# Kernel optimization log

Hardware: AMD Instinct MI355X
Metric: run time of the kernel (lower is better)

Reference implementation:

```python
import jax, jax.numpy as jnp
import numpy as np
import math

CHANNELS = 128
NUM_NODES = 170
LENGTH = 12
BATCH = 128


def setup_inputs() -> dict:
    key = jax.random.key(0)
    k_x, k_es = jax.random.split(key)
    x = jax.random.normal(k_x, (BATCH, CHANNELS, NUM_NODES, LENGTH), dtype=jnp.float32)
    # xavier_uniform for E_s [channels, num_nodes]
    bound = math.sqrt(6.0 / (CHANNELS + NUM_NODES))
    E_s = jax.random.uniform(k_es, (CHANNELS, NUM_NODES), dtype=jnp.float32,
                             minval=-bound, maxval=bound)
    return {"x": x, "E_s": E_s}


def reference(x, E_s):
    # x: [B, C, N, T], E_s: [C, M] with M == N (num_nodes)
    # Note: the original also computes E_t = x * E_tod**2, which is dead code
    # (never used in the returned value), so it is omitted here.
    C = x.shape[1]
    # node embeddings: sum over channel and time -> [B, N, M]
    E_d = jnp.tanh(jnp.einsum('bcnt,cm->bnm', x, E_s))
    # node-node similarity: contract over the M (embedding) axis -> [B, N, N]
    scores = jax.nn.relu(jnp.einsum('bnm,bkm->bnk', E_d, E_d) / jnp.sqrt(jnp.float32(C)))
    A_adp = jax.nn.softmax(scores, axis=-1)  # [B, N, N]
    A_mean = A_adp.mean(axis=0)              # [N, N]
    return (A_mean > 0.5).astype(jnp.float32)
```

## Files before the change

kernel.cpp:

```cpp
#include <hip/hip_runtime.h>
#include <math.h>

#define NB 128
#define NC 128
#define NN 170
#define NT 12
#define MP 176
#define BSROW 196

#define ED_SZ ((size_t)NB * NN * MP)
#define P_SZ  ((size_t)NB * NN * MP)

typedef _Float16 h8 __attribute__((ext_vector_type(8)));
typedef _Float16 h4 __attribute__((ext_vector_type(4)));
typedef __fp16   g2 __attribute__((ext_vector_type(2)));
typedef float    f4 __attribute__((ext_vector_type(4)));

__device__ __forceinline__ float fast_tanh(float x) {
    float cx = fminf(fmaxf(x, -15.f), 15.f);
    float e  = __expf(2.f * cx);
    return (e - 1.f) * __builtin_amdgcn_rcpf(e + 1.f);
}

__global__ __launch_bounds__(256) void k2_fused(const float* __restrict__ x,
                                                const float* __restrict__ Es,
                                                _Float16* __restrict__ Ed) {
    const int b = blockIdx.y, n0 = blockIdx.x * 32;
    const int t = threadIdx.x, tx = t & 15, ty = t >> 4;
    __shared__ __align__(16) float As[16][36];
    __shared__ __align__(16) float Bs[16][BSROW];

    float acc[2][12] = {};
    for (int c0 = 0; c0 < NC; c0 += 16) {
        __syncthreads();
        {
            int c  = t >> 4;
            int nn = (t & 15) * 2;
            #pragma unroll
            for (int u = 0; u < 2; ++u) {
                int n = n0 + nn + u;
                float s = 0.f;
                if (n < NN) {
                    const float4* p = reinterpret_cast<const float4*>(
                        x + ((size_t)((b * NC + c0 + c) * NN) + n) * NT);
                    float4 f0 = p[0], f1 = p[1], f2 = p[2];
                    s = ((f0.x + f0.y) + (f0.z + f0.w))
                      + ((f1.x + f1.y) + (f1.z + f1.w))
                      + ((f2.x + f2.y) + (f2.z + f2.w));
                }
                As[c][nn + u] = s;
            }
        }
        #pragma unroll
        for (int it = 0; it < 11; ++it) {
            int idx = t + it * 256;
            int c = idx / 176, m = idx - c * 176;
            Bs[c][m] = (m < NN) ? Es[(c0 + c) * NN + m] : 0.f;
        }
        __syncthreads();
        #pragma unroll
        for (int cc = 0; cc < 16; ++cc) {
            float2 av = *reinterpret_cast<const float2*>(&As[cc][ty * 2]);
            float a[2] = {av.x, av.y};
            float bb[12];
            #pragma unroll
            for (int off = 0; off < 3; ++off) {
                float4 bv = *reinterpret_cast<const float4*>(&Bs[cc][tx * 4 + off * 64]);
                bb[off * 4 + 0] = bv.x; bb[off * 4 + 1] = bv.y;
                bb[off * 4 + 2] = bv.z; bb[off * 4 + 3] = bv.w;
            }
            #pragma unroll
            for (int ii = 0; ii < 2; ++ii)
                #pragma unroll
                for (int jj = 0; jj < 12; ++jj)
                    acc[ii][jj] = fmaf(a[ii], bb[jj], acc[ii][jj]);
        }
    }
    #pragma unroll
    for (int ii = 0; ii < 2; ++ii) {
        int n = n0 + ty * 2 + ii;
        if (n >= NN) continue;
        _Float16* Erow = Ed + ((size_t)(b * NN + n)) * MP;
        #pragma unroll
        for (int off = 0; off < 3; ++off) {
            int m = tx * 4 + off * 64;
            if (m >= MP) continue;
            g2 lo = __builtin_amdgcn_cvt_pkrtz(fast_tanh(acc[ii][off * 4 + 0]),
                                               fast_tanh(acc[ii][off * 4 + 1]));
            g2 hi = __builtin_amdgcn_cvt_pkrtz(fast_tanh(acc[ii][off * 4 + 2]),
                                               fast_tanh(acc[ii][off * 4 + 3]));
            h4 hv;
            hv[0] = (_Float16)lo[0]; hv[1] = (_Float16)lo[1];
            hv[2] = (_Float16)hi[0]; hv[3] = (_Float16)hi[1];
            *reinterpret_cast<h4*>(Erow + m) = hv;
        }
    }
}

__global__ __launch_bounds__(256) void k3_scores_mfma(const _Float16* __restrict__ Ed,
                                                      _Float16* __restrict__ P) {
    const int b = blockIdx.y, r0 = blockIdx.x * 32;
    const int t = threadIdx.x;
    const int lane = t & 63, wave = t >> 6;
    const int l15 = lane & 15, quad = lane >> 4;

    __shared__ __align__(16) _Float16 Eh[192 * 40];
    __shared__ __align__(16) float    Sc[32 * 204];

    const _Float16* __restrict__ Edb = Ed + (size_t)b * NN * MP;

    f4 acc[2][3] = {};
    for (int mc = 0; mc < 192; mc += 32) {
        __syncthreads();
        #pragma unroll
        for (int it = 0; it < 3; ++it) {
            int idx = t + it * 256;
            int row = idx >> 2, q = idx & 3;
            int col = mc + q * 8;
            h8 v = {};
            if (row < NN && col < MP)
                v = *reinterpret_cast<const h8*>(Edb + (size_t)row * MP + col);
            *reinterpret_cast<h8*>(&Eh[row * 40 + q * 8]) = v;
        }
        __syncthreads();
        const int ko = quad * 8;
        h8 a0 = *reinterpret_cast<const h8*>(&Eh[(r0 + l15) * 40 + ko]);
        h8 a1 = *reinterpret_cast<const h8*>(&Eh[(r0 + 16 + l15) * 40 + ko]);
        #pragma unroll
        for (int ci = 0; ci < 3; ++ci) {
            int kc = (wave * 3 + ci) * 16 + l15;
            h8 bf = *reinterpret_cast<const h8*>(&Eh[kc * 40 + ko]);
            acc[0][ci] = __builtin_amdgcn_mfma_f32_16x16x32_f16(a0, bf, acc[0][ci], 0, 0, 0);
            acc[1][ci] = __builtin_amdgcn_mfma_f32_16x16x32_f16(a1, bf, acc[1][ci], 0, 0, 0);
        }
    }

    const float scale = 0.08838834764831845f;
    #pragma unroll
    for (int rt = 0; rt < 2; ++rt)
        #pragma unroll
        for (int ci = 0; ci < 3; ++ci) {
            int col = (wave * 3 + ci) * 16 + l15;
            #pragma unroll
            for (int reg = 0; reg < 4; ++reg) {
                int rloc = rt * 16 + quad * 4 + reg;
                Sc[rloc * 204 + col] = fmaxf(acc[rt][ci][reg] * scale, 0.f);
            }
        }
    __syncthreads();

    for (int rr = 0; rr < 8; ++rr) {
        int r = wave * 8 + rr;
        int n = r0 + r;
        if (n >= NN) continue;
        float v0 = Sc[r * 204 + lane];
        float v1 = Sc[r * 204 + lane + 64];
        int  k2i = lane + 128;
        bool has2 = (k2i < NN);
        float v2 = has2 ? Sc[r * 204 + k2i] : -1.f;
        float m = fmaxf(fmaxf(v0, v1), v2);
        #pragma unroll
        for (int off = 32; off; off >>= 1) m = fmaxf(m, __shfl_xor(m, off, 64));
        float e0 = __expf(v0 - m);
        float e1 = __expf(v1 - m);
        float e2 = has2 ? __expf(v2 - m) : 0.f;
        float s = e0 + e1 + e2;
        #pragma unroll
        for (int off = 32; off; off >>= 1) s += __shfl_xor(s, off, 64);
        float inv = 1.f / s;
        _Float16* Pr = P + ((size_t)(b * NN + n)) * MP;
        Pr[lane]      = (_Float16)(e0 * inv);
        Pr[lane + 64] = (_Float16)(e1 * inv);
        if (has2) Pr[k2i] = (_Float16)(e2 * inv);
    }
}

__global__ __launch_bounds__(256) void k4_mean_thresh(const _Float16* __restrict__ P,
                                                      float* __restrict__ out) {
    int p = blockIdx.x * 256 + threadIdx.x;
    if (p >= NN * NN) return;
    int n = p / NN, k = p - n * NN;
    const _Float16* base = P + (size_t)n * MP + k;
    float s0 = 0.f, s1 = 0.f, s2 = 0.f, s3 = 0.f;
    #pragma unroll
    for (int b = 0; b < NB; b += 4) {
        s0 += (float)base[(size_t)(b + 0) * NN * MP];
        s1 += (float)base[(size_t)(b + 1) * NN * MP];
        s2 += (float)base[(size_t)(b + 2) * NN * MP];
        s3 += (float)base[(size_t)(b + 3) * NN * MP];
    }
    float s = (s0 + s1) + (s2 + s3);
    out[p] = (s * (1.f / 128.f) > 0.5f) ? 1.f : 0.f;
}

extern "C" void kernel_launch(void* const* d_in, const int* in_sizes, int n_in,
                              void* d_out, int out_size, void* d_ws, size_t ws_size,
                              hipStream_t stream) {
    const float* x  = (const float*)d_in[0];
    const float* Es = (const float*)d_in[1];
    float* out = (float*)d_out;

    _Float16* Ed = (_Float16*)d_ws;
    _Float16* P  = Ed + ED_SZ;

    k2_fused<<<dim3(6, 128), 256, 0, stream>>>(x, Es, Ed);
    k3_scores_mfma<<<dim3(6, 128), 256, 0, stream>>>(Ed, P);
    k4_mean_thresh<<<113, 256, 0, stream>>>(P, out);
}
```

Before: 253.9 us.

## Split time-sum into separate kernel and compute E_d with fp16 MFMA

The fused fp32 FMA kernel for E_d is replaced by three kernels: a transpose and fp16 conversion of E_s, a coalesced kernel that sums x over time into an fp16 buffer, and an MFMA 16x16x32 kernel that computes the channel contraction and applies tanh. The aim is to read x with fully coalesced, simple loads and move the matmul onto matrix cores instead of scalar FMAs. The cost is two extra launches, an extra global round trip for the time-summed x, fp16 rounding of the sums and of E_s, and scalar fp16 stores for E_d.

```diff
diff --git a/kernel.cpp b/kernel.cpp
--- a/kernel.cpp
+++ b/kernel.cpp
@@ -6,10 +6,12 @@
 #define NN 170
 #define NT 12
 #define MP 176
-#define BSROW 196
-
-#define ED_SZ ((size_t)NB * NN * MP)
-#define P_SZ  ((size_t)NB * NN * MP)
+#define MEST 192
+
+#define EST_SZ ((size_t)MEST * NC)
+#define XS_SZ  ((size_t)NB * NC * NN)
+#define ED_SZ  ((size_t)NB * NN * MP)
+#define P_SZ   ((size_t)NB * NN * MP)
 
 typedef _Float16 h8 __attribute__((ext_vector_type(8)));
 typedef _Float16 h4 __attribute__((ext_vector_type(4)));
@@ -22,79 +24,83 @@
     return (e - 1.f) * __builtin_amdgcn_rcpf(e + 1.f);
 }
 
-__global__ __launch_bounds__(256) void k2_fused(const float* __restrict__ x,
-                                                const float* __restrict__ Es,
-                                                _Float16* __restrict__ Ed) {
+__global__ __launch_bounds__(256) void k0t_transpose_es(const float* __restrict__ Es,
+                                                        _Float16* __restrict__ Est) {
+    int idx = blockIdx.x * 256 + threadIdx.x;
+    if (idx >= MEST * NC) return;
+    int m = idx >> 7, c = idx & 127;
+    Est[idx] = (m < NN) ? (_Float16)Es[c * NN + m] : (_Float16)0.f;
+}
+
+__global__ __launch_bounds__(256) void k1_tsum(const float* __restrict__ x,
+                                               _Float16* __restrict__ xs) {
+    unsigned tid = blockIdx.x * 256 + threadIdx.x;
+    unsigned bc = tid / 85u;
+    unsigned p  = tid - bc * 85u;
+    const float4* q = reinterpret_cast<const float4*>(
+        x + (size_t)bc * (NN * NT) + (size_t)p * (2 * NT));
+    float4 f0 = q[0], f1 = q[1], f2 = q[2];
+    float4 f3 = q[3], f4v = q[4], f5 = q[5];
+    float s0 = ((f0.x + f0.y) + (f0.z + f0.w))
+             + ((f1.x + f1.y) + (f1.z + f1.w))
+             + ((f2.x + f2.y) + (f2.z + f2.w));
+    float s1 = ((f3.x + f3.y) + (f3.z + f3.w))
+             + ((f4v.x + f4v.y) + (f4v.z + f4v.w))
+             + ((f5.x + f5.y) + (f5.z + f5.w));
+    g2 pk = __builtin_amdgcn_cvt_pkrtz(s0, s1);
+    *reinterpret_cast<g2*>(xs + (size_t)bc * NN + 2 * p) = pk;
+}
+
+__global__ __launch_bounds__(256) void k2_ed_mfma(const _Float16* __restrict__ xs,
+                                                  const _Float16* __restrict__ Est,
+                                                  _Float16* __restrict__ Ed) {
     const int b = blockIdx.y, n0 = blockIdx.x * 32;
-    const int t = threadIdx.x, tx = t & 15, ty = t >> 4;
-    __shared__ __align__(16) float As[16][36];
-    __shared__ __align__(16) float Bs[16][BSROW];
-
-    float acc[2][12] = {};
-    for (int c0 = 0; c0 < NC; c0 += 16) {
-        __syncthreads();
-        {
-            int c  = t >> 4;
-            int nn = (t & 15) * 2;
+    const int t = threadIdx.x;
+    const int lane = t & 63, wave = t >> 6;
+    const int l15 = lane & 15, quad = lane >> 4;
+
+    __shared__ __align__(16) _Float16 At[32 * 40];
+
+    const _Float16* __restrict__ xsb = xs + (size_t)b * NC * NN;
+
+    f4 acc[2][3] = {};
+    for (int c0 = 0; c0 < NC; c0 += 32) {
+        __syncthreads();
+        #pragma unroll
+        for (int it = 0; it < 4; ++it) {
+            int slot = t + it * 256;
+            int c = slot >> 5, n = slot & 31;
+            _Float16 v = (_Float16)0.f;
+            if (n0 + n < NN)
+                v = xsb[(size_t)(c0 + c) * NN + n0 + n];
+            At[n * 40 + c] = v;
+        }
+        __syncthreads();
+        const int ko = quad * 8;
+        h8 a0 = *reinterpret_cast<const h8*>(&At[l15 * 40 + ko]);
+        h8 a1 = *reinterpret_cast<const h8*>(&At[(16 + l15) * 40 + ko]);
+        #pragma unroll
+        for (int ci = 0; ci < 3; ++ci) {
+            int kc = (wave * 3 + ci) * 16 + l15;
+            h8 bf = *reinterpret_cast<const h8*>(Est + (size_t)kc * NC + c0 + ko);
+            acc[0][ci] = __builtin_amdgcn_mfma_f32_16x16x32_f16(a0, bf, acc[0][ci], 0, 0, 0);
+            acc[1][ci] = __builtin_amdgcn_mfma_f32_16x16x32_f16(a1, bf, acc[1][ci], 0, 0, 0);
+        }
+    }
+
+    #pragma unroll
+    for (int rt = 0; rt < 2; ++rt)
+        #pragma unroll
+        for (int ci = 0; ci < 3; ++ci) {
+            int m = (wave * 3 + ci) * 16 + l15;
+            if (m >= MP) continue;
             #pragma unroll
-            for (int u = 0; u < 2; ++u) {
-                int n = n0 + nn + u;
-                float s = 0.f;
-                if (n < NN) {
-                    const float4* p = reinterpret_cast<const float4*>(
-                        x + ((size_t)((b * NC + c0 + c) * NN) + n) * NT);
-                    float4 f0 = p[0], f1 = p[1], f2 = p[2];
-                    s = ((f0.x + f0.y) + (f0.z + f0.w))
-                      + ((f1.x + f1.y) + (f1.z + f1.w))
-                      + ((f2.x + f2.y) + (f2.z + f2.w));
-                }
-                As[c][nn + u] = s;
+            for (int reg = 0; reg < 4; ++reg) {
+                int n = n0 + rt * 16 + quad * 4 + reg;
+                if (n >= NN) continue;
+                Ed[((size_t)(b * NN + n)) * MP + m] = (_Float16)fast_tanh(acc[rt][ci][reg]);
             }
         }
-        #pragma unroll
-        for (int it = 0; it < 11; ++it) {
-            int idx = t + it * 256;
-            int c = idx / 176, m = idx - c * 176;
-            Bs[c][m] = (m < NN) ? Es[(c0 + c) * NN + m] : 0.f;
-        }
-        __syncthreads();
-        #pragma unroll
-        for (int cc = 0; cc < 16; ++cc) {
-            float2 av = *reinterpret_cast<const float2*>(&As[cc][ty * 2]);
-            float a[2] = {av.x, av.y};
-            float bb[12];
-            #pragma unroll
-            for (int off = 0; off < 3; ++off) {
-                float4 bv = *reinterpret_cast<const float4*>(&Bs[cc][tx * 4 + off * 64]);
-                bb[off * 4 + 0] = bv.x; bb[off * 4 + 1] = bv.y;
-                bb[off * 4 + 2] = bv.z; bb[off * 4 + 3] = bv.w;
-            }
-            #pragma unroll
-            for (int ii = 0; ii < 2; ++ii)
-                #pragma unroll
-                for (int jj = 0; jj < 12; ++jj)
-                    acc[ii][jj] = fmaf(a[ii], bb[jj], acc[ii][jj]);
-        }
-    }
-    #pragma unroll
-    for (int ii = 0; ii < 2; ++ii) {
-        int n = n0 + ty * 2 + ii;
-        if (n >= NN) continue;
-        _Float16* Erow = Ed + ((size_t)(b * NN + n)) * MP;
-        #pragma unroll
-        for (int off = 0; off < 3; ++off) {
-            int m = tx * 4 + off * 64;
-            if (m >= MP) continue;
-            g2 lo = __builtin_amdgcn_cvt_pkrtz(fast_tanh(acc[ii][off * 4 + 0]),
-                                               fast_tanh(acc[ii][off * 4 + 1]));
-            g2 hi = __builtin_amdgcn_cvt_pkrtz(fast_tanh(acc[ii][off * 4 + 2]),
-                                               fast_tanh(acc[ii][off * 4 + 3]));
-            h4 hv;
-            hv[0] = (_Float16)lo[0]; hv[1] = (_Float16)lo[1];
-            hv[2] = (_Float16)hi[0]; hv[3] = (_Float16)hi[1];
-            *reinterpret_cast<h4*>(Erow + m) = hv;
-        }
-    }
 }
 
 __global__ __launch_bounds__(256) void k3_scores_mfma(const _Float16* __restrict__ Ed,
@@ -200,10 +206,14 @@
     const float* Es = (const float*)d_in[1];
     float* out = (float*)d_out;
 
-    _Float16* Ed = (_Float16*)d_ws;
-    _Float16* P  = Ed + ED_SZ;
-
-    k2_fused<<<dim3(6, 128), 256, 0, stream>>>(x, Es, Ed);
+    _Float16* Est = (_Float16*)d_ws;
+    _Float16* xs  = Est + EST_SZ;
+    _Float16* Ed  = xs + XS_SZ;
+    _Float16* P   = Ed + ED_SZ;
+
+    k0t_transpose_es<<<96, 256, 0, stream>>>(Es, Est);
+    k1_tsum<<<5440, 256, 0, stream>>>(x, xs);
+    k2_ed_mfma<<<dim3(6, 128), 256, 0, stream>>>(xs, Est, Ed);
     k3_scores_mfma<<<dim3(6, 128), 256, 0, stream>>>(Ed, P);
     k4_mean_thresh<<<113, 256, 0, stream>>>(P, out);
 }
```

After: 225.1 us. -11.4%, faster.
